# Kernel tuning notes

Hardware: AMD Instinct MI355X
Metric: run time of the kernel (lower is better)

The kernel has to match this reference:

```python
import jax, jax.numpy as jnp
import numpy as np

NUM_CLASSES = 3
NUM_ANCHORS = 3
K = 5 + NUM_CLASSES  # box(4) + obj(1) + classes


def _scale_losses(pred, boxes, labels, pos, neg):
    # pred: [B, A*K, H, W] -> [B, A*H*W, K] matching torch view/permute/view
    B, C, H, W = pred.shape
    p = pred.reshape(B, NUM_ANCHORS, K, H, W).transpose(0, 1, 3, 4, 2).reshape(B, -1, K)
    loc, obj, cls = p[..., :4], p[..., 4], p[..., 5:]
    posf = pos.astype(p.dtype)
    # BCE-with-logits, target = pos_mask: softplus(x) - t*x
    loss_obj = jnp.logaddexp(0.0, obj) - obj * posf  # [B, N]
    num_pos = pos.sum(axis=1)                         # [B] int
    num_neg = jnp.minimum(3 * num_pos, neg.sum(axis=1))
    # hard negative mining: take top-num_neg objectness losses among negatives
    masked = jnp.where(neg, loss_obj, -jnp.inf)
    order = jnp.argsort(-masked, axis=1)
    rank = jnp.argsort(order, axis=1)                 # rank 0 = largest neg loss
    sel = neg & (rank < num_neg[:, None])
    obj_per = (jnp.sum(loss_obj * posf, axis=1) +
               jnp.sum(jnp.where(sel, loss_obj, 0.0), axis=1)) / jnp.maximum(1, num_pos)
    # classification CE, mean over positive anchors
    logp = jax.nn.log_softmax(cls, axis=-1)
    ce = -jnp.take_along_axis(logp, labels[..., None].astype(jnp.int32), axis=-1)[..., 0]
    has_pos = num_pos > 0
    denom = jnp.maximum(num_pos, 1).astype(p.dtype)
    cls_per = jnp.where(has_pos, jnp.sum(ce * posf, axis=1) / denom, 0.0)
    # smooth L1 (beta=1), mean over positive anchors x 4 coords
    d = loc - boxes
    ad = jnp.abs(d)
    sl1 = jnp.where(ad < 1.0, 0.5 * d * d, ad - 0.5)
    loc_per = jnp.where(has_pos,
                        jnp.sum(sl1 * posf[..., None], axis=(1, 2)) / (denom * 4.0), 0.0)
    return obj_per.sum(), cls_per.sum(), loc_per.sum()


def _masks(key, shape):
    u = jax.random.uniform(key, shape)
    pos = u < 0.01
    neg = (~pos) & (u < 0.96)
    return pos, neg


def setup_inputs() -> dict:
    key = jax.random.key(0)
    ks = jax.random.split(key, 12)
    B = 128
    grids = [(80, 80), (40, 40), (20, 20)]
    inp = {}
    for i, (H, W) in enumerate(grids):
        N = NUM_ANCHORS * H * W
        inp[f'pred{i}'] = jax.random.normal(ks[4 * i], (B, NUM_ANCHORS * K, H, W), jnp.float32)
        inp[f'boxes{i}'] = jax.random.uniform(ks[4 * i + 1], (B, N, 4), jnp.float32)
        inp[f'labels{i}'] = jax.random.randint(ks[4 * i + 2], (B, N), 0, NUM_CLASSES, jnp.int32)
        pos, neg = _masks(ks[4 * i + 3], (B, N))
        inp[f'pos{i}'] = pos
        inp[f'neg{i}'] = neg
    return inp


def reference(pred0, pred1, pred2, boxes0, boxes1, boxes2,
              labels0, labels1, labels2, pos0, pos1, pos2, neg0, neg1, neg2):
    B = pred0.shape[0]
    preds = (pred0, pred1, pred2)
    boxes = (boxes0, boxes1, boxes2)
    labels = (labels0, labels1, labels2)
    pos = (pos0, pos1, pos2)
    neg = (neg0, neg1, neg2)
    tot_obj = tot_cls = tot_loc = 0.0
    for s in range(3):
        o, c, l = _scale_losses(preds[s], boxes[s], labels[s], pos[s], neg[s])
        tot_obj = tot_obj + o
        tot_cls = tot_cls + c
        tot_loc = tot_loc + l
    loss_obj = tot_obj / B
    loss_cls = tot_cls / B
    loss_loc = tot_loc / B
    return loss_obj + loss_cls + loss_loc, loss_obj, loss_cls, loss_loc
```

## Files before the change

kernel.cpp:

```cpp
#include <hip/hip_runtime.h>
#include <stdint.h>

#define NA   3
#define KCH  8
#define BLK  512
#define NWV  (BLK / 64)
#define NB   2048
#define MAXN 19200
#define QCAP 512
#define LKEY 0xBFA8u

#define LOG2E 1.4426950408889634f
#define LN2   0.6931471805599453f

struct ScaleParams {
  const float*   pred;
  const float*   boxes;
  const int*     labels;
  const uint8_t* pos;
  const uint8_t* neg;
  int HW;
};

__device__ __forceinline__ float fexp2(float x) { return __builtin_amdgcn_exp2f(x); }
__device__ __forceinline__ float flog2(float x) { return __builtin_amdgcn_logf(x); }

__device__ __forceinline__ float softplus_fast(float x) {
  const float t = fexp2(-fabsf(x) * LOG2E);
  return fmaxf(x, 0.f) + flog2(1.f + t) * LN2;
}

__device__ __forceinline__ float sl1f(float d) {
  float ad = fabsf(d);
  return (ad < 1.f) ? 0.5f * d * d : ad - 0.5f;
}

__device__ __forceinline__ unsigned fkey(unsigned u) {
  return (u & 0x80000000u) ? ~u : (u | 0x80000000u);
}
__device__ __forceinline__ unsigned funkey(unsigned k) {
  return (k & 0x80000000u) ? (k & 0x7FFFFFFFu) : ~k;
}

__device__ __forceinline__ float recon16(unsigned k16) {
  return __uint_as_float(funkey((k16 << 16) | 0x8000u));
}

__device__ __forceinline__ float blockSum(float v, float* scr) {
  #pragma unroll
  for (int off = 32; off > 0; off >>= 1) v += __shfl_down(v, off);
  const int lane = threadIdx.x & 63, w = threadIdx.x >> 6;
  __syncthreads();
  if (lane == 0) scr[w] = v;
  __syncthreads();
  float r = 0.f;
  #pragma unroll
  for (int i = 0; i < NWV; ++i) r += scr[i];
  return r;
}

__device__ __forceinline__ void selectBin1(const unsigned* cb, int krem_in,
    int* iwav, int* sh_dig, int* sh_krem) {
  const int t = threadIdx.x, lane = t & 63, w = t >> 6;
  const int c_t = (int)(cb[0] + cb[1] + cb[2] + cb[3]);
  int ci = c_t;
  #pragma unroll
  for (int off = 1; off < 64; off <<= 1) {
    const int co = __shfl_down(ci, off);
    if (lane + off < 64) ci += co;
  }
  __syncthreads();
  if (lane == 0) iwav[w] = ci;
  __syncthreads();
  int ac = 0;
  #pragma unroll
  for (int w2 = 0; w2 < NWV; ++w2) if (w2 > w) ac += iwav[w2];
  int cum_c = (ci - c_t) + ac;
  #pragma unroll
  for (int q = 3; q >= 0; --q) {
    const int cq = (int)cb[q];
    if (cq > 0 && cum_c < krem_in && krem_in <= cum_c + cq) {
      *sh_dig  = t * 4 + q;
      *sh_krem = krem_in - cum_c;
    }
    cum_c += cq;
  }
  __syncthreads();
}

__global__ void k_zero(unsigned* done) {
  if (threadIdx.x == 0) *done = 0u;
}

struct RowShared {
  unsigned short keys[MAXN];
  unsigned hc[NB];
  int      queue[QCAP];
  int      sh_qn;
  int      iwav[NWV];
  float    fscr[NWV];
  float    wred[NWV][5];
  int      sh_dig, sh_krem;
  float    sh_sa, sh_avg;
  int      sh_flag;
  unsigned c32[32];
  float    s32[32];
};

template<int N>
__device__ __forceinline__ void row_impl(
    const ScaleParams P, int b, float* part, RowShared& S) {
  constexpr int HW = N / 3;
  constexpr int ITER = (N + BLK * 8 - 1) / (BLK * 8);
  const int t = threadIdx.x;

  for (int i = t; i < NB; i += BLK) S.hc[i] = 0u;
  if (t == 0) S.sh_qn = 0;
  __syncthreads();

  const float* predb = P.pred + (size_t)b * (NA * KCH) * HW;
  const size_t row = (size_t)b * N;
  float nneg = 0.f;
  int above = 0;

  float4 o0[ITER], o1[ITER];
  uint2  pmv[ITER], nmv[ITER];
  #pragma unroll
  for (int it = 0; it < ITER; ++it) {
    const int c8 = it * (BLK * 8) + t * 8;
    if (c8 < N) {
      const int a = (c8 >= HW) + (c8 >= 2 * HW);
      const int cell = c8 - a * HW;
      const float* po = predb + (size_t)a * KCH * HW + 4 * HW + cell;
      o0[it]  = *(const float4*)po;
      o1[it]  = *(const float4*)(po + 4);
      pmv[it] = *(const uint2*)(P.pos + row + c8);
      nmv[it] = *(const uint2*)(P.neg + row + c8);
    }
  }

  #pragma unroll
  for (int it = 0; it < ITER; ++it) {
    const int c8 = it * (BLK * 8) + t * 8;
    if (c8 < N) {
      const unsigned long long nm64 =
          ((unsigned long long)nmv[it].y << 32) | nmv[it].x;
      nneg += (float)__popcll(nm64);
      unsigned kk[8];
      #pragma unroll
      for (int q = 0; q < 8; ++q) {
        const float obj = (q < 4) ? (&o0[it].x)[q] : (&o1[it].x)[q - 4];
        const unsigned nm = ((q < 4) ? (nmv[it].x >> (8 * q))
                                     : (nmv[it].y >> (8 * (q - 4)))) & 0xFFu;
        const unsigned pm = ((q < 4) ? (pmv[it].x >> (8 * q))
                                     : (pmv[it].y >> (8 * (q - 4)))) & 0xFFu;
        unsigned k16 = 0u;
        if (nm) {
          k16 = fkey(__float_as_uint(obj)) >> 16;
          if (k16 > LKEY) {
            ++above;
            atomicAdd(&S.hc[k16 >> 5], 1u);
          }
        }
        kk[q] = k16;
        if (pm) {
          const int idx = atomicAdd(&S.sh_qn, 1);
          if (idx < QCAP) S.queue[idx] = c8 + q;
        }
      }
      uint4 kv;
      kv.x = kk[0] | (kk[1] << 16); kv.y = kk[2] | (kk[3] << 16);
      kv.z = kk[4] | (kk[5] << 16); kv.w = kk[6] | (kk[7] << 16);
      *reinterpret_cast<uint4*>(&S.keys[c8]) = kv;
    }
  }
  __syncthreads();
  const int npos = S.sh_qn;
  const int qn = min(npos, QCAP);

  float posobj = 0.f, ce = 0.f, loc = 0.f;
  for (int i = t; i < qn; i += BLK) {
    const int j = S.queue[i];
    const int a = (j >= HW) + (j >= 2 * HW);
    const int cell = j - a * HW;
    const float* pa = predb + (size_t)a * KCH * HW;
    posobj += softplus_fast(-pa[4 * HW + cell]);
    const float c0f = pa[5 * HW + cell];
    const float c1f = pa[6 * HW + cell];
    const float c2f = pa[7 * HW + cell];
    const float m = fmaxf(fmaxf(c0f, c1f), c2f);
    const float e = fexp2((c0f - m) * LOG2E) + fexp2((c1f - m) * LOG2E)
                  + fexp2((c2f - m) * LOG2E);
    const float lse = m + flog2(e) * LN2;
    const int lab = P.labels[row + j];
    ce += lse - ((lab == 0) ? c0f : (lab == 1) ? c1f : c2f);
    const float4 bx = *(const float4*)(P.boxes + (size_t)(row + j) * 4);
    loc += sl1f(pa[0 * HW + cell] - bx.x) + sl1f(pa[1 * HW + cell] - bx.y)
         + sl1f(pa[2 * HW + cell] - bx.z) + sl1f(pa[3 * HW + cell] - bx.w);
  }

  {
    float v[5] = {nneg, posobj, ce, loc, (float)above};
    #pragma unroll
    for (int i = 0; i < 5; ++i) {
      #pragma unroll
      for (int off = 32; off > 0; off >>= 1) v[i] += __shfl_down(v[i], off);
    }
    const int lane = t & 63, w = t >> 6;
    __syncthreads();
    if (lane == 0) {
      #pragma unroll
      for (int i = 0; i < 5; ++i) S.wred[w][i] = v[i];
    }
    __syncthreads();
  }
  float red[5];
  #pragma unroll
  for (int i = 0; i < 5; ++i) {
    float acc = 0.f;
    #pragma unroll
    for (int w2 = 0; w2 < NWV; ++w2) acc += S.wred[w2][i];
    red[i] = acc;
  }
  const float t_po = red[1], t_ce = red[2], t_lc = red[3];
  const int t_above = (int)red[4];
  const int k = min(3 * npos, (int)red[0]);

  float sel = 0.f;
  if (k > 0) {
    unsigned Lcur = LKEY;
    if (t_above < k) {
      #pragma unroll
      for (int it = 0; it < ITER; ++it) {
        const int c8 = it * (BLK * 8) + t * 8;
        if (c8 < N) {
          const uint4 kv = *reinterpret_cast<const uint4*>(&S.keys[c8]);
          const unsigned ks[8] = {kv.x & 0xFFFFu, kv.x >> 16, kv.y & 0xFFFFu,
                                  kv.y >> 16,     kv.z & 0xFFFFu, kv.z >> 16,
                                  kv.w & 0xFFFFu, kv.w >> 16};
          #pragma unroll
          for (int q = 0; q < 8; ++q)
            if (ks[q] && ks[q] <= LKEY) atomicAdd(&S.hc[ks[q] >> 5], 1u);
        }
      }
      __syncthreads();
      Lcur = 0u;
    }

    unsigned cb[4];
    #pragma unroll
    for (int q = 0; q < 4; ++q) cb[q] = S.hc[4 * t + q];
    selectBin1(cb, k, S.iwav, &S.sh_dig, &S.sh_krem);
    const int bin1 = S.sh_dig; const int krem1 = S.sh_krem;

    if (t < 32) { S.c32[t] = 0u; S.s32[t] = 0.f; }
    __syncthreads();

    float sgt = 0.f;
    #pragma unroll
    for (int it = 0; it < ITER; ++it) {
      const int c8 = it * (BLK * 8) + t * 8;
      if (c8 < N) {
        const uint4 kv = *reinterpret_cast<const uint4*>(&S.keys[c8]);
        const unsigned ks[8] = {kv.x & 0xFFFFu, kv.x >> 16, kv.y & 0xFFFFu,
                                kv.y >> 16,     kv.z & 0xFFFFu, kv.z >> 16,
                                kv.w & 0xFFFFu, kv.w >> 16};
        #pragma unroll
        for (int q = 0; q < 8; ++q) {
          const unsigned k16 = ks[q];
          if (!k16) continue;
          const int kb = (int)(k16 >> 5);
          if (kb > bin1) sgt += softplus_fast(recon16(k16));
          else if (kb == bin1 && k16 > Lcur) {
            atomicAdd(&S.c32[k16 & 31u], 1u);
            atomicAdd(&S.s32[k16 & 31u], softplus_fast(recon16(k16)));
          }
        }
      }
    }
    __syncthreads();
    const float t_sgt = blockSum(sgt, S.fscr);

    if (t < 64) {
      const int cc = (t < 32) ? (int)S.c32[t] : 0;
      const float ss = (t < 32) ? S.s32[t] : 0.f;
      int ci = cc; float si = ss;
      #pragma unroll
      for (int off = 1; off < 64; off <<= 1) {
        const int   co = __shfl_down(ci, off);
        const float so = __shfl_down(si, off);
        if ((t & 63) + off < 64) { ci += co; si += so; }
      }
      const int   above_c = ci - cc;
      const float above_s = si - ss;
      if (t < 32 && cc > 0 && above_c < krem1 && krem1 <= above_c + cc) {
        S.sh_krem = krem1 - above_c;
        S.sh_sa   = t_sgt + above_s;
        S.sh_avg  = ss / (float)cc;
      }
    }
    __syncthreads();
    sel = S.sh_sa + (float)S.sh_krem * S.sh_avg;
  }

  if (t == 0) {
    const float denom = (float)max(npos, 1);
    part[0] = (t_po + sel) / denom;
    part[1] = (npos > 0) ? t_ce / denom : 0.f;
    part[2] = (npos > 0) ? t_lc / (denom * 4.f) : 0.f;
  }
}

__global__ __launch_bounds__(BLK) void k_row(
    ScaleParams p0, ScaleParams p1, ScaleParams p2,
    int B, int R, float invB, float* g_part, unsigned* done, float* out) {
  __shared__ RowShared S;
  const int r = blockIdx.x;
  const int s = (r >= B) + (r >= 2 * B);
  const int b = r - s * B;
  float* part = g_part + (size_t)r * 4;
  if (s == 0)      row_impl<19200>(p0, b, part, S);
  else if (s == 1) row_impl<4800>(p1, b, part, S);
  else             row_impl<1200>(p2, b, part, S);

  if (threadIdx.x == 0) {
    __threadfence();
    const unsigned old = atomicAdd(done, 1u);
    S.sh_flag = (old == (unsigned)(R - 1)) ? 1 : 0;
  }
  __syncthreads();
  if (S.sh_flag) {
    __threadfence();
    const int t = threadIdx.x;
    float o = 0.f, c = 0.f, l = 0.f;
    for (int i = t; i < R; i += BLK) {
      o += g_part[i * 4 + 0];
      c += g_part[i * 4 + 1];
      l += g_part[i * 4 + 2];
    }
    o = blockSum(o, S.fscr);
    c = blockSum(c, S.fscr);
    l = blockSum(l, S.fscr);
    if (t == 0) {
      out[0] = (o + c + l) * invB;
      out[1] = o * invB;
      out[2] = c * invB;
      out[3] = l * invB;
    }
  }
}

extern "C" void kernel_launch(void* const* d_in, const int* in_sizes, int n_in,
                              void* d_out, int out_size, void* d_ws, size_t ws_size,
                              hipStream_t stream) {
  (void)n_in; (void)out_size; (void)ws_size;

  const int HW0 = 80 * 80, HW1 = 40 * 40, HW2 = 20 * 20;
  const int B = in_sizes[0] / (NA * KCH * HW0);
  const int R = 3 * B;
  const float invB = 1.f / (float)B;

  ScaleParams p0{(const float*)d_in[0],  (const float*)d_in[1],
                 (const int*)d_in[2],    (const uint8_t*)d_in[3],
                 (const uint8_t*)d_in[4], HW0};
  ScaleParams p1{(const float*)d_in[5],  (const float*)d_in[6],
                 (const int*)d_in[7],    (const uint8_t*)d_in[8],
                 (const uint8_t*)d_in[9], HW1};
  ScaleParams p2{(const float*)d_in[10], (const float*)d_in[11],
                 (const int*)d_in[12],   (const uint8_t*)d_in[13],
                 (const uint8_t*)d_in[14], HW2};

  float* out = (float*)d_out;
  unsigned* done = (unsigned*)d_ws;
  float* g_part = (float*)((char*)d_ws + 256);

  k_zero<<<1, 64, 0, stream>>>(done);
  k_row<<<R, BLK, 0, stream>>>(p0, p1, p2, B, R, invB, g_part, done, out);
}
```

Measured before the change: 26.72 us.

## Replace per-row LDS key array with compacted candidate list and sum histogram

Instead of storing a 16-bit key for every anchor in LDS (38 KB), only keys above the pre-threshold are appended to a small compact buffer, and the coarse histogram also accumulates softplus sums per bin. The sum above the selected bin then comes directly from the histogram prefix scan, so the second pass over keys only touches the compacted candidates. Rare fallbacks (too few candidates or overflow) re-read the predictions from global memory. The smaller LDS footprint should allow more blocks per CU. In exchange, every candidate now does an extra float atomic and a softplus evaluation during the first pass.

```diff
diff --git a/kernel.cpp b/kernel.cpp
--- a/kernel.cpp
+++ b/kernel.cpp
@@ -6,8 +6,8 @@
 #define BLK  512
 #define NWV  (BLK / 64)
 #define NB   2048
-#define MAXN 19200
 #define QCAP 512
+#define CCAP 4096
 #define LKEY 0xBFA8u
 
 #define LOG2E 1.4426950408889634f
@@ -41,65 +41,20 @@
 __device__ __forceinline__ unsigned funkey(unsigned k) {
   return (k & 0x80000000u) ? (k & 0x7FFFFFFFu) : ~k;
 }
-
-__device__ __forceinline__ float recon16(unsigned k16) {
-  return __uint_as_float(funkey((k16 << 16) | 0x8000u));
-}
-
-__device__ __forceinline__ float blockSum(float v, float* scr) {
-  #pragma unroll
-  for (int off = 32; off > 0; off >>= 1) v += __shfl_down(v, off);
-  const int lane = threadIdx.x & 63, w = threadIdx.x >> 6;
-  __syncthreads();
-  if (lane == 0) scr[w] = v;
-  __syncthreads();
-  float r = 0.f;
-  #pragma unroll
-  for (int i = 0; i < NWV; ++i) r += scr[i];
-  return r;
-}
-
-__device__ __forceinline__ void selectBin1(const unsigned* cb, int krem_in,
-    int* iwav, int* sh_dig, int* sh_krem) {
-  const int t = threadIdx.x, lane = t & 63, w = t >> 6;
-  const int c_t = (int)(cb[0] + cb[1] + cb[2] + cb[3]);
-  int ci = c_t;
-  #pragma unroll
-  for (int off = 1; off < 64; off <<= 1) {
-    const int co = __shfl_down(ci, off);
-    if (lane + off < 64) ci += co;
-  }
-  __syncthreads();
-  if (lane == 0) iwav[w] = ci;
-  __syncthreads();
-  int ac = 0;
-  #pragma unroll
-  for (int w2 = 0; w2 < NWV; ++w2) if (w2 > w) ac += iwav[w2];
-  int cum_c = (ci - c_t) + ac;
-  #pragma unroll
-  for (int q = 3; q >= 0; --q) {
-    const int cq = (int)cb[q];
-    if (cq > 0 && cum_c < krem_in && krem_in <= cum_c + cq) {
-      *sh_dig  = t * 4 + q;
-      *sh_krem = krem_in - cum_c;
-    }
-    cum_c += cq;
-  }
-  __syncthreads();
-}
-
-__global__ void k_zero(unsigned* done) {
-  if (threadIdx.x == 0) *done = 0u;
-}
-
-struct RowShared {
-  unsigned short keys[MAXN];
+__device__ __forceinline__ float sp16(unsigned k16) {
+  return softplus_fast(__uint_as_float(funkey((k16 << 16) | 0x8000u)));
+}
+
+struct __align__(16) RowShared {
+  unsigned short compact[CCAP];
   unsigned hc[NB];
+  float    hs[NB];
   int      queue[QCAP];
-  int      sh_qn;
+  int      sh_qn, sh_nc;
   int      iwav[NWV];
+  float    fwav[NWV];
   float    fscr[NWV];
-  float    wred[NWV][5];
+  float    wred[NWV][4];
   int      sh_dig, sh_krem;
   float    sh_sa, sh_avg;
   int      sh_flag;
@@ -107,21 +62,125 @@
   float    s32[32];
 };
 
-template<int N>
+__device__ __forceinline__ float blockSum(float v, float* scr) {
+  #pragma unroll
+  for (int off = 32; off > 0; off >>= 1) v += __shfl_down(v, off);
+  const int lane = threadIdx.x & 63, w = threadIdx.x >> 6;
+  __syncthreads();
+  if (lane == 0) scr[w] = v;
+  __syncthreads();
+  float r = 0.f;
+  #pragma unroll
+  for (int i = 0; i < NWV; ++i) r += scr[i];
+  return r;
+}
+
+__device__ __forceinline__ void selectDigit4(const unsigned* cb, const float* sb,
+                                             int krem_in, RowShared& S) {
+  const int t = threadIdx.x, lane = t & 63, w = t >> 6;
+  int c_t = 0; float s_t = 0.f;
+  #pragma unroll
+  for (int q = 0; q < 4; ++q) { c_t += (int)cb[q]; s_t += sb[q]; }
+  int ci = c_t; float si = s_t;
+  #pragma unroll
+  for (int off = 1; off < 64; off <<= 1) {
+    const int   co = __shfl_down(ci, off);
+    const float so = __shfl_down(si, off);
+    if (lane + off < 64) { ci += co; si += so; }
+  }
+  __syncthreads();
+  if (lane == 0) { S.iwav[w] = ci; S.fwav[w] = si; }
+  __syncthreads();
+  int ac = 0; float as = 0.f;
+  #pragma unroll
+  for (int w2 = 0; w2 < NWV; ++w2)
+    if (w2 > w) { ac += S.iwav[w2]; as += S.fwav[w2]; }
+  int   cum_c = (ci - c_t) + ac;
+  float cum_s = (si - s_t) + as;
+  #pragma unroll
+  for (int q = 3; q >= 0; --q) {
+    const int cq = (int)cb[q];
+    if (cq > 0 && cum_c < krem_in && krem_in <= cum_c + cq) {
+      S.sh_dig  = t * 4 + q;
+      S.sh_krem = krem_in - cum_c;
+      S.sh_sa   = cum_s;
+    }
+    cum_c += cq; cum_s += sb[q];
+  }
+  __syncthreads();
+}
+
+template<int HW>
+__device__ void hist_low(const ScaleParams& P, int b, RowShared& S) {
+  constexpr int N = 3 * HW;
+  const float* predb = P.pred + (size_t)b * (NA * KCH) * HW;
+  const size_t row = (size_t)b * N;
+  for (int c8 = threadIdx.x * 8; c8 < N; c8 += BLK * 8) {
+    const int a = (c8 >= HW) + (c8 >= 2 * HW);
+    const int cell = c8 - a * HW;
+    const float* po = predb + (size_t)a * KCH * HW + 4 * HW + cell;
+    const float4 o0 = *(const float4*)po;
+    const float4 o1 = *(const float4*)(po + 4);
+    const uint2 nmv = *(const uint2*)(P.neg + row + c8);
+    #pragma unroll
+    for (int q = 0; q < 8; ++q) {
+      const unsigned nm = ((q < 4) ? (nmv.x >> (8 * q))
+                                   : (nmv.y >> (8 * (q - 4)))) & 0xFFu;
+      if (nm) {
+        const float obj = (q < 4) ? (&o0.x)[q] : (&o1.x)[q - 4];
+        const unsigned k16 = fkey(__float_as_uint(obj)) >> 16;
+        if (k16 <= LKEY) {
+          atomicAdd(&S.hc[k16 >> 5], 1u);
+          atomicAdd(&S.hs[k16 >> 5], sp16(k16));
+        }
+      }
+    }
+  }
+}
+
+template<int HW>
+__device__ void refine_global(const ScaleParams& P, int b, int bin1,
+                              unsigned lmin, RowShared& S) {
+  constexpr int N = 3 * HW;
+  const float* predb = P.pred + (size_t)b * (NA * KCH) * HW;
+  const size_t row = (size_t)b * N;
+  for (int c8 = threadIdx.x * 8; c8 < N; c8 += BLK * 8) {
+    const int a = (c8 >= HW) + (c8 >= 2 * HW);
+    const int cell = c8 - a * HW;
+    const float* po = predb + (size_t)a * KCH * HW + 4 * HW + cell;
+    const float4 o0 = *(const float4*)po;
+    const float4 o1 = *(const float4*)(po + 4);
+    const uint2 nmv = *(const uint2*)(P.neg + row + c8);
+    #pragma unroll
+    for (int q = 0; q < 8; ++q) {
+      const unsigned nm = ((q < 4) ? (nmv.x >> (8 * q))
+                                   : (nmv.y >> (8 * (q - 4)))) & 0xFFu;
+      if (nm) {
+        const float obj = (q < 4) ? (&o0.x)[q] : (&o1.x)[q - 4];
+        const unsigned k16 = fkey(__float_as_uint(obj)) >> 16;
+        if (k16 > lmin && (int)(k16 >> 5) == bin1) {
+          atomicAdd(&S.c32[k16 & 31u], 1u);
+          atomicAdd(&S.s32[k16 & 31u], sp16(k16));
+        }
+      }
+    }
+  }
+}
+
+template<int HW>
 __device__ __forceinline__ void row_impl(
     const ScaleParams P, int b, float* part, RowShared& S) {
-  constexpr int HW = N / 3;
+  constexpr int N = 3 * HW;
   constexpr int ITER = (N + BLK * 8 - 1) / (BLK * 8);
   const int t = threadIdx.x;
 
-  for (int i = t; i < NB; i += BLK) S.hc[i] = 0u;
-  if (t == 0) S.sh_qn = 0;
+  for (int i = t; i < NB; i += BLK) { S.hc[i] = 0u; S.hs[i] = 0.f; }
+  if (t == 0) { S.sh_qn = 0; S.sh_nc = 0; }
   __syncthreads();
 
   const float* predb = P.pred + (size_t)b * (NA * KCH) * HW;
   const size_t row = (size_t)b * N;
   float nneg = 0.f;
-  int above = 0;
 
   float4 o0[ITER], o1[ITER];
   uint2  pmv[ITER], nmv[ITER];
@@ -146,36 +205,32 @@
       const unsigned long long nm64 =
           ((unsigned long long)nmv[it].y << 32) | nmv[it].x;
       nneg += (float)__popcll(nm64);
-      unsigned kk[8];
       #pragma unroll
       for (int q = 0; q < 8; ++q) {
-        const float obj = (q < 4) ? (&o0[it].x)[q] : (&o1[it].x)[q - 4];
         const unsigned nm = ((q < 4) ? (nmv[it].x >> (8 * q))
                                      : (nmv[it].y >> (8 * (q - 4)))) & 0xFFu;
         const unsigned pm = ((q < 4) ? (pmv[it].x >> (8 * q))
                                      : (pmv[it].y >> (8 * (q - 4)))) & 0xFFu;
-        unsigned k16 = 0u;
         if (nm) {
-          k16 = fkey(__float_as_uint(obj)) >> 16;
+          const float obj = (q < 4) ? (&o0[it].x)[q] : (&o1[it].x)[q - 4];
+          const unsigned k16 = fkey(__float_as_uint(obj)) >> 16;
           if (k16 > LKEY) {
-            ++above;
+            const int ci = atomicAdd(&S.sh_nc, 1);
+            if (ci < CCAP) S.compact[ci] = (unsigned short)k16;
             atomicAdd(&S.hc[k16 >> 5], 1u);
+            atomicAdd(&S.hs[k16 >> 5], sp16(k16));
           }
         }
-        kk[q] = k16;
         if (pm) {
           const int idx = atomicAdd(&S.sh_qn, 1);
           if (idx < QCAP) S.queue[idx] = c8 + q;
         }
       }
-      uint4 kv;
-      kv.x = kk[0] | (kk[1] << 16); kv.y = kk[2] | (kk[3] << 16);
-      kv.z = kk[4] | (kk[5] << 16); kv.w = kk[6] | (kk[7] << 16);
-      *reinterpret_cast<uint4*>(&S.keys[c8]) = kv;
     }
   }
   __syncthreads();
   const int npos = S.sh_qn;
+  const int nc   = S.sh_nc;
   const int qn = min(npos, QCAP);
 
   float posobj = 0.f, ce = 0.f, loc = 0.f;
@@ -200,9 +255,9 @@
   }
 
   {
-    float v[5] = {nneg, posobj, ce, loc, (float)above};
+    float v[4] = {nneg, posobj, ce, loc};
     #pragma unroll
-    for (int i = 0; i < 5; ++i) {
+    for (int i = 0; i < 4; ++i) {
       #pragma unroll
       for (int off = 32; off > 0; off >>= 1) v[i] += __shfl_down(v[i], off);
     }
@@ -210,76 +265,53 @@
     __syncthreads();
     if (lane == 0) {
       #pragma unroll
-      for (int i = 0; i < 5; ++i) S.wred[w][i] = v[i];
+      for (int i = 0; i < 4; ++i) S.wred[w][i] = v[i];
     }
     __syncthreads();
   }
-  float red[5];
-  #pragma unroll
-  for (int i = 0; i < 5; ++i) {
+  float red[4];
+  #pragma unroll
+  for (int i = 0; i < 4; ++i) {
     float acc = 0.f;
     #pragma unroll
     for (int w2 = 0; w2 < NWV; ++w2) acc += S.wred[w2][i];
     red[i] = acc;
   }
   const float t_po = red[1], t_ce = red[2], t_lc = red[3];
-  const int t_above = (int)red[4];
   const int k = min(3 * npos, (int)red[0]);
 
   float sel = 0.f;
   if (k > 0) {
-    unsigned Lcur = LKEY;
-    if (t_above < k) {
-      #pragma unroll
-      for (int it = 0; it < ITER; ++it) {
-        const int c8 = it * (BLK * 8) + t * 8;
-        if (c8 < N) {
-          const uint4 kv = *reinterpret_cast<const uint4*>(&S.keys[c8]);
-          const unsigned ks[8] = {kv.x & 0xFFFFu, kv.x >> 16, kv.y & 0xFFFFu,
-                                  kv.y >> 16,     kv.z & 0xFFFFu, kv.z >> 16,
-                                  kv.w & 0xFFFFu, kv.w >> 16};
-          #pragma unroll
-          for (int q = 0; q < 8; ++q)
-            if (ks[q] && ks[q] <= LKEY) atomicAdd(&S.hc[ks[q] >> 5], 1u);
-        }
-      }
+    unsigned lmin = LKEY;
+    const bool fell = (nc < k);
+    if (fell) {
+      hist_low<HW>(P, b, S);
       __syncthreads();
-      Lcur = 0u;
-    }
-
-    unsigned cb[4];
+      lmin = 0u;
+    }
+
+    unsigned cb[4]; float sb[4];
     #pragma unroll
-    for (int q = 0; q < 4; ++q) cb[q] = S.hc[4 * t + q];
-    selectBin1(cb, k, S.iwav, &S.sh_dig, &S.sh_krem);
+    for (int q = 0; q < 4; ++q) { cb[q] = S.hc[4*t+q]; sb[q] = S.hs[4*t+q]; }
+    selectDigit4(cb, sb, k, S);
     const int bin1 = S.sh_dig; const int krem1 = S.sh_krem;
+    const float sa1 = S.sh_sa;
 
     if (t < 32) { S.c32[t] = 0u; S.s32[t] = 0.f; }
     __syncthreads();
 
-    float sgt = 0.f;
-    #pragma unroll
-    for (int it = 0; it < ITER; ++it) {
-      const int c8 = it * (BLK * 8) + t * 8;
-      if (c8 < N) {
-        const uint4 kv = *reinterpret_cast<const uint4*>(&S.keys[c8]);
-        const unsigned ks[8] = {kv.x & 0xFFFFu, kv.x >> 16, kv.y & 0xFFFFu,
-                                kv.y >> 16,     kv.z & 0xFFFFu, kv.z >> 16,
-                                kv.w & 0xFFFFu, kv.w >> 16};
-        #pragma unroll
-        for (int q = 0; q < 8; ++q) {
-          const unsigned k16 = ks[q];
-          if (!k16) continue;
-          const int kb = (int)(k16 >> 5);
-          if (kb > bin1) sgt += softplus_fast(recon16(k16));
-          else if (kb == bin1 && k16 > Lcur) {
-            atomicAdd(&S.c32[k16 & 31u], 1u);
-            atomicAdd(&S.s32[k16 & 31u], softplus_fast(recon16(k16)));
-          }
+    if (!fell && nc <= CCAP) {
+      for (int i = t; i < nc; i += BLK) {
+        const unsigned k16 = S.compact[i];
+        if ((int)(k16 >> 5) == bin1) {
+          atomicAdd(&S.c32[k16 & 31u], 1u);
+          atomicAdd(&S.s32[k16 & 31u], sp16(k16));
         }
       }
+    } else {
+      refine_global<HW>(P, b, bin1, lmin, S);
     }
     __syncthreads();
-    const float t_sgt = blockSum(sgt, S.fscr);
 
     if (t < 64) {
       const int cc = (t < 32) ? (int)S.c32[t] : 0;
@@ -295,7 +327,7 @@
       const float above_s = si - ss;
       if (t < 32 && cc > 0 && above_c < krem1 && krem1 <= above_c + cc) {
         S.sh_krem = krem1 - above_c;
-        S.sh_sa   = t_sgt + above_s;
+        S.sh_sa   = sa1 + above_s;
         S.sh_avg  = ss / (float)cc;
       }
     }
@@ -309,6 +341,10 @@
     part[1] = (npos > 0) ? t_ce / denom : 0.f;
     part[2] = (npos > 0) ? t_lc / (denom * 4.f) : 0.f;
   }
+}
+
+__global__ void k_zero(unsigned* done) {
+  if (threadIdx.x == 0) *done = 0u;
 }
 
 __global__ __launch_bounds__(BLK) void k_row(
@@ -319,9 +355,9 @@
   const int s = (r >= B) + (r >= 2 * B);
   const int b = r - s * B;
   float* part = g_part + (size_t)r * 4;
-  if (s == 0)      row_impl<19200>(p0, b, part, S);
-  else if (s == 1) row_impl<4800>(p1, b, part, S);
-  else             row_impl<1200>(p2, b, part, S);
+  if (s == 0)      row_impl<6400>(p0, b, part, S);
+  else if (s == 1) row_impl<1600>(p1, b, part, S);
+  else             row_impl<400>(p2, b, part, S);
 
   if (threadIdx.x == 0) {
     __threadfence();
```

New measurement: 28.74 us. 1.08x slower.
